# Optimization experiments

Measured on AMD Instinct MI355X. Metric: run time of the kernel, lower is better.

## Reference

```python
import jax, jax.numpy as jnp
import numpy as np
from jax import lax

DIM = 512
MED = 2 * DIM            # expansion_ratio * dim
NF = 4                   # num_filters
SIZE = 64                # spatial size (H = W = size)
FS = SIZE // 2 + 1       # rfft filter size
HR = int(0.5 * DIM)      # reweight hidden (NNConv, 1x1 convs)
HS = int(0.5 * DIM)      # spatial_reweight hidden (Convs, 3x3 convs)
B = 16


def _conv1x1(x, w, b):
    # x: [B,C,H,W], w: [O,C,1,1]
    return jnp.einsum('bchw,oc->bohw', x, w[:, :, 0, 0]) + b[None, :, None, None]


def _conv3x3(x, w, b):
    # x: [B,C,H,W], w: [O,C,3,3], padding=1
    return lax.conv_general_dilated(x, w, (1, 1), 'SAME') + b[None, :, None, None]


def setup_inputs() -> dict:
    key = jax.random.key(0)
    ks = jax.random.split(key, 12)
    n = lambda k, shape, s=0.02: jax.random.normal(k, shape, jnp.float32) * s
    return dict(
        x=jax.random.normal(ks[0], (B, DIM, SIZE, SIZE), jnp.float32),
        w_pw1=n(ks[1], (MED, DIM)),                 # pwconv1 (Linear, no bias)
        w_pw2=n(ks[2], (DIM, MED)),                 # pwconv2 (Linear, no bias)
        star_scale=jnp.ones((1,), jnp.float32),     # StarReLU scale
        star_bias=jnp.zeros((1,), jnp.float32),     # StarReLU bias
        rw_fc1_w=n(ks[3], (HR, DIM, 1, 1)), rw_fc1_b=jnp.zeros((HR,), jnp.float32),
        rw_conv_w=n(ks[4], (HR, HR, 1, 1)), rw_conv_b=jnp.zeros((HR,), jnp.float32),
        rw_fc2_w=n(ks[5], (NF * MED, HR, 1, 1)), rw_fc2_b=jnp.zeros((NF * MED,), jnp.float32),
        sp_fc1_w=n(ks[6], (HS, DIM, 3, 3)), sp_fc1_b=jnp.zeros((HS,), jnp.float32),
        sp_fc2_w=n(ks[7], (NF * MED, HS, 3, 3)), sp_fc2_b=jnp.zeros((NF * MED,), jnp.float32),
        complex_weights=n(ks[8], (SIZE, FS, NF, 2), 0.02),
        spatial_weights=n(ks[9], (SIZE, SIZE, NF), 0.03),
    )


def reference(x, w_pw1, w_pw2, star_scale, star_bias,
              rw_fc1_w, rw_fc1_b, rw_conv_w, rw_conv_b, rw_fc2_w, rw_fc2_b,
              sp_fc1_w, sp_fc1_b, sp_fc2_w, sp_fc2_b,
              complex_weights, spatial_weights):
    Bn, _, H, W = x.shape
    # --- routing branch (NNConv: 1x1 conv -> relu -> 1x1 conv -> relu -> 1x1 conv) ---
    r = jax.nn.relu(_conv1x1(x, rw_fc1_w, rw_fc1_b))
    r = jax.nn.relu(_conv1x1(r, rw_conv_w, rw_conv_b))
    r = _conv1x1(r, rw_fc2_w, rw_fc2_b)                      # [B, NF*MED, H, W]
    routeing = jax.nn.softmax(r.mean(axis=(2, 3)).reshape(Bn, NF, MED), axis=1)
    # --- spatial routing branch (Convs: 3x3 conv -> relu -> 3x3 conv) ---
    s = jax.nn.relu(_conv3x3(x, sp_fc1_w, sp_fc1_b))
    s = _conv3x3(s, sp_fc2_w, sp_fc2_b)                      # [B, NF*MED, H, W]
    spatial_routeing = jax.nn.softmax(s.mean(axis=(2, 3)).reshape(Bn, NF, MED), axis=1)
    # --- main path ---
    xc = jnp.transpose(x, (0, 2, 3, 1))                      # [B,H,W,DIM]
    xp = jnp.einsum('bhwc,mc->bhwm', xc, w_pw1)              # pwconv1 -> [B,H,W,MED]
    xp = star_scale * jnp.square(jax.nn.relu(xp)) + star_bias  # StarReLU
    xf = jnp.fft.rfft2(xp, axes=(1, 2), norm='ortho')        # [B,H,FS,MED] complex64
    cw = lax.complex(complex_weights[..., 0], complex_weights[..., 1])  # [H,FS,NF]
    weight = jnp.einsum('bfc,hwf->bhwc', routeing.astype(cw.dtype), cw)  # [B,H,FS,MED]
    spatial_weight = jnp.einsum('bfc,hwf->bhwc', spatial_routeing, spatial_weights)  # [B,H,W,MED]
    xs = jnp.fft.irfft2(xf * weight, s=(H, W), axes=(1, 2), norm='ortho')
    out = xp * spatial_weight + xs                            # spatial gating + FFT filter
    out = jnp.einsum('bhwm,dm->bhwd', out, w_pw2)             # pwconv2
    return jnp.transpose(out, (0, 3, 1, 2))                   # [B,DIM,H,W]
```

## Files before the change

kernel.cpp:

```cpp
#include <hip/hip_runtime.h>

#define HW    4096
#define DIMC  512
#define MEDC  1024
#define HRC   256
#define HSC   256
#define NBATCH 16

typedef __attribute__((ext_vector_type(8))) short bf16x8;
typedef __attribute__((ext_vector_type(4))) float f32x4;

static const size_t R1_OFF    = 0;
static const size_t XT_OFF    = 8388608;
static const size_t WCONV_OFF = 25165824;
static const size_t WR1_OFF   = 25755648;
static const size_t WRC_OFF   = 25821184;
static const size_t XP_OFF    = 0;
static const size_t WB1_OFF   = 67108864;
static const size_t WB2_OFF   = 67371008;
static const size_t MEAN_OFF  = 67633152;
static const size_t AGG_OFF   = MEAN_OFF + 4096;
static const size_t TAP_OFF   = AGG_OFF + 36864;
static const size_t ROUTE_OFF = TAP_OFF + 36864;
static const size_t SR_OFF    = ROUTE_OFF + 65536;
static const size_t WS_END    = SR_OFF + 65536;

__device__ __forceinline__ unsigned short f2bf(float f) {
  unsigned u = __float_as_uint(f);
  unsigned r = (u + 0x7fffu + ((u >> 16) & 1u)) >> 16;
  return (unsigned short)r;
}

__global__ __launch_bounds__(256) void cvt_bf16(
    const float* __restrict__ src, unsigned short* __restrict__ dst, int n)
{
  int i = blockIdx.x * 256 + threadIdx.x;
  if (i < n) dst[i] = f2bf(src[i]);
}

__global__ __launch_bounds__(256) void xpose_bf16(
    const float* __restrict__ x, unsigned short* __restrict__ xT)
{
  __shared__ unsigned short T[32][33];
  const int tid = threadIdx.x;
  const int p0 = blockIdx.x * 32, c0 = blockIdx.y * 32, bb = blockIdx.z;
#pragma unroll
  for (int i = 0; i < 4; i++) {
    int idx = i * 256 + tid;
    int c_l = idx >> 5, p_l = idx & 31;
    T[c_l][p_l] = f2bf(x[((size_t)(bb * DIMC + c0 + c_l)) * HW + p0 + p_l]);
  }
  __syncthreads();
#pragma unroll
  for (int i = 0; i < 4; i++) {
    int idx = i * 256 + tid;
    int p_l = idx >> 5, c_l = idx & 31;
    xT[((size_t)bb * HW + p0 + p_l) * DIMC + c0 + c_l] = T[c_l][p_l];
  }
}

__global__ __launch_bounds__(256) void wconv_bf16(
    const float* __restrict__ w, unsigned short* __restrict__ wbf)
{
  int idx = blockIdx.x * 256 + threadIdx.x;
  if (idx < HSC * DIMC) {
#pragma unroll
    for (int t = 0; t < 9; t++)
      wbf[(size_t)t * (HSC * DIMC) + idx] = f2bf(w[(size_t)idx * 9 + t]);
  }
}

template<int EPI, int ASRC>
__global__ __launch_bounds__(256) void gemm_bf16(
    const void* __restrict__ Aptr, const unsigned short* __restrict__ Wb,
    const float* __restrict__ bias, float* __restrict__ Cf,
    unsigned short* __restrict__ Cb, float* __restrict__ meansum,
    const float* __restrict__ star_scale, const float* __restrict__ star_bias,
    int K, int Ntot)
{
  __shared__ __align__(16) unsigned short As[128 * 40];
  __shared__ __align__(16) unsigned short Bs[128 * 40];
  const int tid = threadIdx.x;
  const int pix0 = blockIdx.x * 128;
  const int n0g = blockIdx.y * 128;
  const int bb = blockIdx.z;
  const int wid = tid >> 6, lane = tid & 63;
  const int lo = lane & 15, hi = lane >> 4;
  const int wm = wid >> 1, wn = wid & 1;

  f32x4 acc[4][4];
#pragma unroll
  for (int mi = 0; mi < 4; mi++)
#pragma unroll
    for (int ni = 0; ni < 4; ni++) acc[mi][ni] = (f32x4){0.f, 0.f, 0.f, 0.f};

  const int nsteps = K >> 5;
  for (int s = 0; s < nsteps; s++) {
    const int c0 = s * 32;
    if (ASRC == 0) {
      const unsigned short* AT = (const unsigned short*)Aptr;
#pragma unroll
      for (int it = 0; it < 2; it++) {
        int idx = it * 256 + tid;
        int p = idx >> 2, co = (idx & 3) * 8;
        uint4 v = *(const uint4*)&AT[((size_t)bb * HW + pix0 + p) * K + c0 + co];
        *(uint4*)&As[p * 40 + co] = v;
      }
    } else {
      const float* Af = (const float*)Aptr;
#pragma unroll
      for (int it = 0; it < 16; it++) {
        int idx = it * 256 + tid;
        int k_l = idx >> 7, p_l = idx & 127;
        float v = Af[((size_t)bb * K + c0 + k_l) * HW + pix0 + p_l];
        As[p_l * 40 + k_l] = f2bf(v);
      }
    }
#pragma unroll
    for (int it = 0; it < 2; it++) {
      int idx = it * 256 + tid;
      int o = idx >> 2, co = (idx & 3) * 8;
      uint4 v = *(const uint4*)&Wb[(size_t)(n0g + o) * K + c0 + co];
      *(uint4*)&Bs[o * 40 + co] = v;
    }
    __syncthreads();

    bf16x8 a[4], bq[4];
#pragma unroll
    for (int mi = 0; mi < 4; mi++)
      a[mi] = *(const bf16x8*)&As[(wm * 64 + mi * 16 + lo) * 40 + hi * 8];
#pragma unroll
    for (int ni = 0; ni < 4; ni++)
      bq[ni] = *(const bf16x8*)&Bs[(wn * 64 + ni * 16 + lo) * 40 + hi * 8];
#pragma unroll
    for (int mi = 0; mi < 4; mi++)
#pragma unroll
      for (int ni = 0; ni < 4; ni++)
        acc[mi][ni] = __builtin_amdgcn_mfma_f32_16x16x32_bf16(a[mi], bq[ni], acc[mi][ni], 0, 0, 0);
    __syncthreads();
  }

  if (EPI == 3) {
#pragma unroll
    for (int ni = 0; ni < 4; ni++) {
      const int n = n0g + wn * 64 + ni * 16 + lo;
      const float bia = bias[n];
      float T = 0.f;
#pragma unroll
      for (int mi = 0; mi < 4; mi++)
#pragma unroll
        for (int r = 0; r < 4; r++)
          T += fmaxf(acc[mi][ni][r] + bia, 0.f);
      T += __shfl_xor(T, 16);
      T += __shfl_xor(T, 32);
      if (hi == 0) atomicAdd(&meansum[bb * Ntot + n], T);
    }
    return;
  }

  if (EPI == 1) {
#pragma unroll
    for (int ni = 0; ni < 4; ni++) {
      const int n = n0g + wn * 64 + ni * 16 + lo;
      const float bia = bias[n];
#pragma unroll
      for (int mi = 0; mi < 4; mi++)
#pragma unroll
        for (int r = 0; r < 4; r++) {
          const int pix = pix0 + wm * 64 + mi * 16 + hi * 4 + r;
          Cb[((size_t)bb * HW + pix) * Ntot + n] = f2bf(fmaxf(acc[mi][ni][r] + bia, 0.f));
        }
    }
    return;
  }

  float ss = 1.f, sb = 0.f;
  if (EPI == 2) { ss = star_scale[0]; sb = star_bias[0]; }
#pragma unroll
  for (int ni = 0; ni < 4; ni++) {
    const int n = n0g + wn * 64 + ni * 16 + lo;
#pragma unroll
    for (int mi = 0; mi < 4; mi++) {
      const int pixb = pix0 + wm * 64 + mi * 16 + hi * 4;
      float4 v;
      float* vv = (float*)&v;
#pragma unroll
      for (int r = 0; r < 4; r++) {
        float t = acc[mi][ni][r];
        if (EPI == 2) { t = fmaxf(t, 0.f); t = ss * t * t + sb; }
        vv[r] = t;
      }
      *(float4*)&Cf[((size_t)bb * Ntot + n) * HW + pixb] = v;
    }
  }
}

__global__ __launch_bounds__(256) void conv3_mfma(
    const unsigned short* __restrict__ xT, const unsigned short* __restrict__ wbf,
    const float* __restrict__ bias, float* __restrict__ agg)
{
  __shared__ __align__(16) unsigned short As[128 * 40];
  __shared__ __align__(16) unsigned short Bs[128 * 40];
  const int tid = threadIdx.x;
  const int bx = blockIdx.x;
  const int n0g = blockIdx.y * 128;
  const int bb = blockIdx.z;
  const int h0 = bx * 2;
  const int wid = tid >> 6;
  const int lane = tid & 63;
  const int lo = lane & 15, hi = lane >> 4;
  const int wm = wid >> 1;
  const int wn = wid & 1;

  f32x4 acc[4][4];
#pragma unroll
  for (int mi = 0; mi < 4; mi++)
#pragma unroll
    for (int ni = 0; ni < 4; ni++) acc[mi][ni] = (f32x4){0.f, 0.f, 0.f, 0.f};

  for (int s = 0; s < 144; s++) {
    const int t = s >> 4;
    const int c0 = (s & 15) * 32;
    const int di = t / 3 - 1, dj = t % 3 - 1;
#pragma unroll
    for (int it = 0; it < 2; it++) {
      int idx = it * 256 + tid;
      int pix = idx >> 2, co = (idx & 3) * 8;
      int h = h0 + (pix >> 6) + di;
      int col = (pix & 63) + dj;
      uint4 v = make_uint4(0u, 0u, 0u, 0u);
      if (h >= 0 && h < 64 && col >= 0 && col < 64)
        v = *(const uint4*)&xT[((size_t)bb * HW + h * 64 + col) * DIMC + c0 + co];
      *(uint4*)&As[pix * 40 + co] = v;
    }
#pragma unroll
    for (int it = 0; it < 2; it++) {
      int idx = it * 256 + tid;
      int o = idx >> 2, co = (idx & 3) * 8;
      uint4 v = *(const uint4*)&wbf[((size_t)t * (HSC * DIMC)) + (size_t)(n0g + o) * DIMC + c0 + co];
      *(uint4*)&Bs[o * 40 + co] = v;
    }
    __syncthreads();

    bf16x8 a[4], bfr[4];
#pragma unroll
    for (int mi = 0; mi < 4; mi++)
      a[mi] = *(const bf16x8*)&As[(wm * 64 + mi * 16 + lo) * 40 + hi * 8];
#pragma unroll
    for (int ni = 0; ni < 4; ni++)
      bfr[ni] = *(const bf16x8*)&Bs[(wn * 64 + ni * 16 + lo) * 40 + hi * 8];
#pragma unroll
    for (int mi = 0; mi < 4; mi++)
#pragma unroll
      for (int ni = 0; ni < 4; ni++)
        acc[mi][ni] = __builtin_amdgcn_mfma_f32_16x16x32_bf16(a[mi], bfr[ni], acc[mi][ni], 0, 0, 0);
    __syncthreads();
  }

  const int h = h0 + wm;
#pragma unroll
  for (int ni = 0; ni < 4; ni++) {
    const int o = n0g + wn * 64 + ni * 16 + lo;
    const float bia = bias[o];
    float T = 0.f;
#pragma unroll
    for (int mi = 0; mi < 4; mi++)
#pragma unroll
      for (int r = 0; r < 4; r++)
        T += fmaxf(acc[mi][ni][r] + bia, 0.f);
    T += __shfl_xor(T, 16);
    T += __shfl_xor(T, 32);
    float* ag = &agg[((size_t)bb * HSC + o) * 9];
    if (hi == 0) {
      atomicAdd(ag + 0, T);
      if (h == 0)  atomicAdd(ag + 1, T);
      if (h == 63) atomicAdd(ag + 2, T);
      float c0v = fmaxf(acc[0][ni][0] + bia, 0.f);
      atomicAdd(ag + 3, c0v);
      if (h == 0)  atomicAdd(ag + 5, c0v);
      if (h == 63) atomicAdd(ag + 7, c0v);
    }
    if (hi == 3) {
      float cwv = fmaxf(acc[3][ni][3] + bia, 0.f);
      atomicAdd(ag + 4, cwv);
      if (h == 0)  atomicAdd(ag + 6, cwv);
      if (h == 63) atomicAdd(ag + 8, cwv);
    }
  }
}

__global__ void tap_compute(const float* __restrict__ agg, float* __restrict__ tap)
{
  int b = blockIdx.x; int c = threadIdx.x;
  const float* a = &agg[((size_t)b * HSC + c) * 9];
  float T = a[0], R0 = a[1], RH = a[2], C0 = a[3], CW = a[4];
  float s00 = a[5], s0W = a[6], sH0 = a[7], sHW = a[8];
  float* tp = &tap[((size_t)b * HSC + c) * 9];
#pragma unroll
  for (int i = 0; i < 3; i++)
#pragma unroll
    for (int j = 0; j < 3; j++) {
      int di = i - 1, dj = j - 1;
      float v = T;
      if (di == -1) v -= RH; else if (di == 1) v -= R0;
      if (dj == -1) v -= CW; else if (dj == 1) v -= C0;
      if (di == -1 && dj == -1) v += sHW;
      if (di == -1 && dj ==  1) v += sH0;
      if (di ==  1 && dj == -1) v += s0W;
      if (di ==  1 && dj ==  1) v += s00;
      tp[i * 3 + j] = v * (1.f / 4096.f);
    }
}

__global__ __launch_bounds__(256) void route_softmax(
    const float* __restrict__ meansum, const float* __restrict__ W,
    const float* __restrict__ bias, float* __restrict__ route)
{
  __shared__ float mv[HRC];
  int b = blockIdx.y;
  int m = blockIdx.x * 256 + threadIdx.x;
  mv[threadIdx.x] = meansum[b * HRC + threadIdx.x] * (1.f / 4096.f);
  __syncthreads();
  float l[4];
#pragma unroll
  for (int f = 0; f < 4; f++) {
    int o = f * MEDC + m;
    float accv = bias[o];
    const float* wr = &W[(size_t)o * HRC];
    for (int c = 0; c < HRC; c++) accv += wr[c] * mv[c];
    l[f] = accv;
  }
  float mx = fmaxf(fmaxf(l[0], l[1]), fmaxf(l[2], l[3]));
  float e[4], s = 0.f;
#pragma unroll
  for (int f = 0; f < 4; f++) { e[f] = expf(l[f] - mx); s += e[f]; }
  float inv = 1.f / s;
#pragma unroll
  for (int f = 0; f < 4; f++) route[((size_t)b * 4 + f) * MEDC + m] = e[f] * inv;
}

__global__ __launch_bounds__(256) void sproute_softmax(
    const float* __restrict__ tap, const float* __restrict__ W,
    const float* __restrict__ bias, float* __restrict__ sroute)
{
  __shared__ float tv[HSC * 9];
  int b = blockIdx.y;
  int m = blockIdx.x * 256 + threadIdx.x;
#pragma unroll
  for (int i = 0; i < 9; i++) {
    int idx = i * 256 + threadIdx.x;
    tv[idx] = tap[(size_t)b * HSC * 9 + idx];
  }
  __syncthreads();
  float l[4];
#pragma unroll
  for (int f = 0; f < 4; f++) {
    int o = f * MEDC + m;
    float accv = bias[o];
    const float* wr = &W[(size_t)o * HSC * 9];
    for (int ct = 0; ct < HSC * 9; ct++) accv += wr[ct] * tv[ct];
    l[f] = accv;
  }
  float mx = fmaxf(fmaxf(l[0], l[1]), fmaxf(l[2], l[3]));
  float e[4], s = 0.f;
#pragma unroll
  for (int f = 0; f < 4; f++) { e[f] = expf(l[f] - mx); s += e[f]; }
  float inv = 1.f / s;
#pragma unroll
  for (int f = 0; f < 4; f++) sroute[((size_t)b * 4 + f) * MEDC + m] = e[f] * inv;
}

template<int SGN>
__device__ __forceinline__ void dft8(const float* xr, const float* xi, float* Xr, float* Xi) {
  const float S = (float)SGN;
  const float r = 0.70710678118654752440f;
  float t0r = xr[0] + xr[4], t0i = xi[0] + xi[4];
  float t1r = xr[0] - xr[4], t1i = xi[0] - xi[4];
  float t2r = xr[2] + xr[6], t2i = xi[2] + xi[6];
  float t3r = xr[2] - xr[6], t3i = xi[2] - xi[6];
  float E0r = t0r + t2r, E0i = t0i + t2i;
  float E2r = t0r - t2r, E2i = t0i - t2i;
  float E1r = t1r - S * t3i, E1i = t1i + S * t3r;
  float E3r = t1r + S * t3i, E3i = t1i - S * t3r;
  float u0r = xr[1] + xr[5], u0i = xi[1] + xi[5];
  float u1r = xr[1] - xr[5], u1i = xi[1] - xi[5];
  float u2r = xr[3] + xr[7], u2i = xi[3] + xi[7];
  float u3r = xr[3] - xr[7], u3i = xi[3] - xi[7];
  float O0r = u0r + u2r, O0i = u0i + u2i;
  float O2r = u0r - u2r, O2i = u0i - u2i;
  float O1r = u1r - S * u3i, O1i = u1i + S * u3r;
  float O3r = u1r + S * u3i, O3i = u1i - S * u3r;
  float p1r = r * (O1r - S * O1i), p1i = r * (S * O1r + O1i);
  float p2r = -S * O2i,            p2i = S * O2r;
  float p3r = -r * (O3r + S * O3i), p3i = r * (S * O3r - O3i);
  Xr[0] = E0r + O0r; Xi[0] = E0i + O0i;
  Xr[4] = E0r - O0r; Xi[4] = E0i - O0i;
  Xr[1] = E1r + p1r; Xi[1] = E1i + p1i;
  Xr[5] = E1r - p1r; Xi[5] = E1i - p1i;
  Xr[2] = E2r + p2r; Xi[2] = E2i + p2i;
  Xr[6] = E2r - p2r; Xi[6] = E2i - p2i;
  Xr[3] = E3r + p3r; Xi[3] = E3i + p3i;
  Xr[7] = E3r - p3r; Xi[7] = E3i - p3i;
}

__global__ __launch_bounds__(256) void fft_filter(
    float* __restrict__ xp, const float* __restrict__ route,
    const float* __restrict__ sroute, const float* __restrict__ cw,
    const float* __restrict__ spw)
{
  __shared__ float Fr[64][34], Fi[64][34];
  __shared__ float Cr[2176], Ci[2176];
  __shared__ float twc[64], tws[64];
  const int tid = threadIdx.x;
  const int blk = blockIdx.x;
  const int b = blk >> 10;
  const int m = blk & 1023;
  float* img = xp + (size_t)blk * HW;

  if (tid < 64) {
    float ang = (2.f * 3.14159265358979323846f / 64.f) * (float)tid;
    twc[tid] = cosf(ang); tws[tid] = sinf(ang);
  }
  float r4[4], s4[4];
#pragma unroll
  for (int f = 0; f < 4; f++) {
    r4[f] = route[((size_t)b * 4 + f) * MEDC + m] * (1.f / 4096.f);
    s4[f] = sroute[((size_t)b * 4 + f) * MEDC + m];
  }
  __syncthreads();

#pragma unroll
  for (int half = 0; half < 2; half++) {
    {
      const int rh = tid & 31, n2 = tid >> 5;
      const int r = rh + half * 32;
      float xr[8], xi[8], Br[8], Bi[8];
#pragma unroll
      for (int n1 = 0; n1 < 8; n1++) { xr[n1] = img[r * 64 + 8 * n1 + n2]; xi[n1] = 0.f; }
      dft8<-1>(xr, xi, Br, Bi);
#pragma unroll
      for (int k1 = 0; k1 < 8; k1++) {
        int a = n2 * k1;
        float c = twc[a], s = tws[a];
        Cr[rh * 67 + k1 * 8 + n2] = Br[k1] * c + Bi[k1] * s;
        Ci[rh * 67 + k1 * 8 + n2] = Bi[k1] * c - Br[k1] * s;
      }
    }
    __syncthreads();
    {
      const int rh = tid & 31, k1 = tid >> 5;
      const int r = rh + half * 32;
      float xr[8], xi[8], Xr[8], Xi[8];
#pragma unroll
      for (int n2 = 0; n2 < 8; n2++) {
        xr[n2] = Cr[rh * 67 + k1 * 8 + n2];
        xi[n2] = Ci[rh * 67 + k1 * 8 + n2];
      }
      dft8<-1>(xr, xi, Xr, Xi);
      const int kmax = (k1 == 0) ? 5 : 4;
#pragma unroll
      for (int k2 = 0; k2 < 5; k2++) {
        if (k2 < kmax) {
          Fr[r][k1 + 8 * k2] = Xr[k2];
          Fi[r][k1 + 8 * k2] = Xi[k2];
        }
      }
    }
    __syncthreads();
  }

  for (int t = tid; t < 264; t += 256) {
    const int k = t % 33, n2 = t / 33;
    float xr[8], xi[8], Br[8], Bi[8];
#pragma unroll
    for (int n1 = 0; n1 < 8; n1++) { xr[n1] = Fr[8 * n1 + n2][k]; xi[n1] = Fi[8 * n1 + n2][k]; }
    dft8<-1>(xr, xi, Br, Bi);
#pragma unroll
    for (int k1 = 0; k1 < 8; k1++) {
      int a = n2 * k1;
      float c = twc[a], s = tws[a];
      Cr[(k1 * 8 + n2) * 34 + k] = Br[k1] * c + Bi[k1] * s;
      Ci[(k1 * 8 + n2) * 34 + k] = Bi[k1] * c - Br[k1] * s;
    }
  }
  __syncthreads();
  for (int t = tid; t < 264; t += 256) {
    const int k = t % 33, k1 = t / 33;
    float xr[8], xi[8], Xr[8], Xi[8];
#pragma unroll
    for (int n2 = 0; n2 < 8; n2++) {
      xr[n2] = Cr[(k1 * 8 + n2) * 34 + k];
      xi[n2] = Ci[(k1 * 8 + n2) * 34 + k];
    }
    dft8<-1>(xr, xi, Xr, Xi);
#pragma unroll
    for (int k2 = 0; k2 < 8; k2++) {
      const int kh = k1 + 8 * k2;
      const float* cwp = &cw[(size_t)(kh * 33 + k) * 8];
      float wre = r4[0] * cwp[0] + r4[1] * cwp[2] + r4[2] * cwp[4] + r4[3] * cwp[6];
      float wim = r4[0] * cwp[1] + r4[1] * cwp[3] + r4[2] * cwp[5] + r4[3] * cwp[7];
      Fr[kh][k] = Xr[k2] * wre - Xi[k2] * wim;
      Fi[kh][k] = Xr[k2] * wim + Xi[k2] * wre;
    }
  }
  __syncthreads();

  for (int t = tid; t < 264; t += 256) {
    const int k = t % 33, m2 = t / 33;
    float xr[8], xi[8], Br[8], Bi[8];
#pragma unroll
    for (int m1 = 0; m1 < 8; m1++) { xr[m1] = Fr[8 * m1 + m2][k]; xi[m1] = Fi[8 * m1 + m2][k]; }
    dft8<1>(xr, xi, Br, Bi);
#pragma unroll
    for (int h1 = 0; h1 < 8; h1++) {
      int a = m2 * h1;
      float c = twc[a], s = tws[a];
      Cr[(h1 * 8 + m2) * 34 + k] = Br[h1] * c - Bi[h1] * s;
      Ci[(h1 * 8 + m2) * 34 + k] = Bi[h1] * c + Br[h1] * s;
    }
  }
  __syncthreads();
  for (int t = tid; t < 264; t += 256) {
    const int k = t % 33, h1 = t / 33;
    float xr[8], xi[8], Xr[8], Xi[8];
#pragma unroll
    for (int m2 = 0; m2 < 8; m2++) {
      xr[m2] = Cr[(h1 * 8 + m2) * 34 + k];
      xi[m2] = Ci[(h1 * 8 + m2) * 34 + k];
    }
    dft8<1>(xr, xi, Xr, Xi);
#pragma unroll
    for (int h2 = 0; h2 < 8; h2++) {
      Fr[h1 + 8 * h2][k] = Xr[h2];
      Fi[h1 + 8 * h2][k] = Xi[h2];
    }
  }
  __syncthreads();

#pragma unroll
  for (int half = 0; half < 2; half++) {
    {
      const int rh = tid & 31, m2 = tid >> 5;
      const int r = rh + half * 32;
      float xr[8], xi[8], Br[8], Bi[8];
      if (m2 == 0) {
        xr[0] = Fr[r][0];  xi[0] = 0.f;
        xr[4] = Fr[r][32]; xi[4] = 0.f;
      } else {
        xr[0] = 2.f * Fr[r][m2]; xi[0] = 2.f * Fi[r][m2];
        xr[4] = 0.f; xi[4] = 0.f;
      }
#pragma unroll
      for (int m1 = 1; m1 < 4; m1++) {
        xr[m1] = 2.f * Fr[r][8 * m1 + m2];
        xi[m1] = 2.f * Fi[r][8 * m1 + m2];
      }
      xr[5] = 0.f; xi[5] = 0.f; xr[6] = 0.f; xi[6] = 0.f; xr[7] = 0.f; xi[7] = 0.f;
      dft8<1>(xr, xi, Br, Bi);
#pragma unroll
      for (int h1 = 0; h1 < 8; h1++) {
        int a = m2 * h1;
        float c = twc[a], s = tws[a];
        Cr[rh * 67 + h1 * 8 + m2] = Br[h1] * c - Bi[h1] * s;
        Ci[rh * 67 + h1 * 8 + m2] = Bi[h1] * c + Br[h1] * s;
      }
    }
    __syncthreads();
    {
      const int rh = tid & 31, h1 = tid >> 5;
      const int r = rh + half * 32;
      float xr[8], xi[8], Xr[8], Xi[8];
#pragma unroll
      for (int m2 = 0; m2 < 8; m2++) {
        xr[m2] = Cr[rh * 67 + h1 * 8 + m2];
        xi[m2] = Ci[rh * 67 + h1 * 8 + m2];
      }
      dft8<1>(xr, xi, Xr, Xi);
#pragma unroll
      for (int h2 = 0; h2 < 8; h2++) {
        const int w = h1 + 8 * h2;
        const int pix = r * 64 + w;
        float xv = img[pix];
        const float* sp = &spw[(size_t)pix * 4];
        float sw = s4[0] * sp[0] + s4[1] * sp[1] + s4[2] * sp[2] + s4[3] * sp[3];
        img[pix] = xv * sw + Xr[h2];
      }
    }
    __syncthreads();
  }
}

extern "C" void kernel_launch(void* const* d_in, const int* in_sizes, int n_in,
                              void* d_out, int out_size, void* d_ws, size_t ws_size,
                              hipStream_t stream) {
  const float* x          = (const float*)d_in[0];
  const float* w_pw1      = (const float*)d_in[1];
  const float* w_pw2      = (const float*)d_in[2];
  const float* star_scale = (const float*)d_in[3];
  const float* star_bias  = (const float*)d_in[4];
  const float* rw1w = (const float*)d_in[5];
  const float* rw1b = (const float*)d_in[6];
  const float* rwcw = (const float*)d_in[7];
  const float* rwcb = (const float*)d_in[8];
  const float* rw2w = (const float*)d_in[9];
  const float* rw2b = (const float*)d_in[10];
  const float* sp1w = (const float*)d_in[11];
  const float* sp1b = (const float*)d_in[12];
  const float* sp2w = (const float*)d_in[13];
  const float* sp2b = (const float*)d_in[14];
  const float* cw   = (const float*)d_in[15];
  const float* spw  = (const float*)d_in[16];

  if (ws_size < WS_END * sizeof(float)) return;

  float* ws = (float*)d_ws;
  float* xp = ws + XP_OFF;
  unsigned short* r1    = (unsigned short*)(ws + R1_OFF);
  unsigned short* xT    = (unsigned short*)(ws + XT_OFF);
  unsigned short* wconv = (unsigned short*)(ws + WCONV_OFF);
  unsigned short* wr1   = (unsigned short*)(ws + WR1_OFF);
  unsigned short* wrc   = (unsigned short*)(ws + WRC_OFF);
  unsigned short* wb1   = (unsigned short*)(ws + WB1_OFF);
  unsigned short* wb2   = (unsigned short*)(ws + WB2_OFF);
  float* meansum = ws + MEAN_OFF;
  float* agg     = ws + AGG_OFF;
  float* tap     = ws + TAP_OFF;
  float* route   = ws + ROUTE_OFF;
  float* sr      = ws + SR_OFF;
  float* out = (float*)d_out;

  hipMemsetAsync(meansum, 0, (4096 + 36864) * sizeof(float), stream);

  xpose_bf16<<<dim3(128, 16, 16), 256, 0, stream>>>(x, xT);
  wconv_bf16<<<512, 256, 0, stream>>>(sp1w, wconv);
  cvt_bf16<<<2048, 256, 0, stream>>>(w_pw1, wb1, MEDC * DIMC);
  cvt_bf16<<<2048, 256, 0, stream>>>(w_pw2, wb2, DIMC * MEDC);
  cvt_bf16<<<512, 256, 0, stream>>>(rw1w, wr1, HRC * DIMC);
  cvt_bf16<<<256, 256, 0, stream>>>(rwcw, wrc, HRC * HRC);

  gemm_bf16<1, 0><<<dim3(32, 2, 16), 256, 0, stream>>>(
      xT, wr1, rw1b, nullptr, r1, nullptr, nullptr, nullptr, DIMC, HRC);
  gemm_bf16<3, 0><<<dim3(32, 2, 16), 256, 0, stream>>>(
      r1, wrc, rwcb, nullptr, nullptr, meansum, nullptr, nullptr, HRC, HRC);
  route_softmax<<<dim3(4, 16), 256, 0, stream>>>(meansum, rw2w, rw2b, route);

  conv3_mfma<<<dim3(32, 2, 16), 256, 0, stream>>>(xT, wconv, sp1b, agg);
  tap_compute<<<16, 256, 0, stream>>>(agg, tap);
  sproute_softmax<<<dim3(4, 16), 256, 0, stream>>>(tap, sp2w, sp2b, sr);

  gemm_bf16<2, 1><<<dim3(32, 8, 16), 256, 0, stream>>>(
      x, wb1, nullptr, xp, nullptr, nullptr, star_scale, star_bias, DIMC, MEDC);
  fft_filter<<<16384, 256, 0, stream>>>(xp, route, sr, cw, spw);
  gemm_bf16<0, 1><<<dim3(32, 4, 16), 256, 0, stream>>>(
      xp, wb2, nullptr, out, nullptr, nullptr, nullptr, nullptr, MEDC, DIMC);
}
```

Measured before the change: 1.727 ms.

## Restructure FFT filter to one wavefront with register-resident 64-point FFTs

Rewrites the per-image FFT filter so a single 64-thread wave handles each image, with every lane holding a full 64-point row or column in registers and running a register-only 8x8 decomposition. The old version used 256 threads, separate real/imag shared arrays and many intermediate shared round-trips. The new one keeps only one float2 spectrum buffer in shared memory and uses vectorized float4 global loads and stores. This cuts barriers and shared traffic, but needs about 128+ registers per thread, which may spill or limit occupancy. In the column pass only 33 of 64 lanes do work, so half the wave idles.

New measurement: 2.280 ms. +32.0%, slower.

```diff
diff --git a/kernel.cpp b/kernel.cpp
--- a/kernel.cpp
+++ b/kernel.cpp
@@ -403,23 +403,70 @@
   Xr[7] = E3r - p3r; Xi[7] = E3i - p3i;
 }
 
-__global__ __launch_bounds__(256) void fft_filter(
+template<int SGN>
+__device__ __forceinline__ void dft8_strided(float* xr, float* xi, const int base, const int stride) {
+  float ar[8], ai[8], Br[8], Bi[8];
+#pragma unroll
+  for (int j = 0; j < 8; j++) { ar[j] = xr[base + j * stride]; ai[j] = xi[base + j * stride]; }
+  dft8<SGN>(ar, ai, Br, Bi);
+#pragma unroll
+  for (int j = 0; j < 8; j++) { xr[base + j * stride] = Br[j]; xi[base + j * stride] = Bi[j]; }
+}
+
+template<int SGN>
+__device__ __forceinline__ void fft64_n2r(float* xr, float* xi, const float2* tw) {
+#pragma unroll
+  for (int g = 0; g < 8; g++) dft8_strided<SGN>(xr, xi, g, 8);
+#pragma unroll
+  for (int s = 0; s < 64; s++) {
+    const int a = (s >> 3) * (s & 7);
+    if (a) {
+      float2 t = tw[a];
+      float c = t.x, si = (float)SGN * t.y;
+      float rr = xr[s] * c - xi[s] * si;
+      xi[s] = xr[s] * si + xi[s] * c;
+      xr[s] = rr;
+    }
+  }
+#pragma unroll
+  for (int g = 0; g < 8; g++) dft8_strided<SGN>(xr, xi, 8 * g, 1);
+}
+
+template<int SGN>
+__device__ __forceinline__ void fft64_r2n(float* xr, float* xi, const float2* tw) {
+#pragma unroll
+  for (int g = 0; g < 8; g++) dft8_strided<SGN>(xr, xi, 8 * g, 1);
+#pragma unroll
+  for (int s = 0; s < 64; s++) {
+    const int a = (s >> 3) * (s & 7);
+    if (a) {
+      float2 t = tw[a];
+      float c = t.x, si = (float)SGN * t.y;
+      float rr = xr[s] * c - xi[s] * si;
+      xi[s] = xr[s] * si + xi[s] * c;
+      xr[s] = rr;
+    }
+  }
+#pragma unroll
+  for (int g = 0; g < 8; g++) dft8_strided<SGN>(xr, xi, g, 8);
+}
+
+__global__ __launch_bounds__(64, 2) void fft_filter(
     float* __restrict__ xp, const float* __restrict__ route,
     const float* __restrict__ sroute, const float* __restrict__ cw,
     const float* __restrict__ spw)
 {
-  __shared__ float Fr[64][34], Fi[64][34];
-  __shared__ float Cr[2176], Ci[2176];
-  __shared__ float twc[64], tws[64];
-  const int tid = threadIdx.x;
+  __shared__ float2 Fs[64 * 33];
+  __shared__ float2 tw[64];
+  const int lane = threadIdx.x;
   const int blk = blockIdx.x;
   const int b = blk >> 10;
   const int m = blk & 1023;
   float* img = xp + (size_t)blk * HW;
 
-  if (tid < 64) {
-    float ang = (2.f * 3.14159265358979323846f / 64.f) * (float)tid;
-    twc[tid] = cosf(ang); tws[tid] = sinf(ang);
+  {
+    float ang = (6.28318530717958647693f / 64.f) * (float)lane;
+    tw[lane] = make_float2(cosf(ang), sinf(ang));
   }
   float r4[4], s4[4];
 #pragma unroll
@@ -429,164 +476,75 @@
   }
   __syncthreads();
 
-#pragma unroll
-  for (int half = 0; half < 2; half++) {
-    {
-      const int rh = tid & 31, n2 = tid >> 5;
-      const int r = rh + half * 32;
-      float xr[8], xi[8], Br[8], Bi[8];
-#pragma unroll
-      for (int n1 = 0; n1 < 8; n1++) { xr[n1] = img[r * 64 + 8 * n1 + n2]; xi[n1] = 0.f; }
-      dft8<-1>(xr, xi, Br, Bi);
-#pragma unroll
-      for (int k1 = 0; k1 < 8; k1++) {
-        int a = n2 * k1;
-        float c = twc[a], s = tws[a];
-        Cr[rh * 67 + k1 * 8 + n2] = Br[k1] * c + Bi[k1] * s;
-        Ci[rh * 67 + k1 * 8 + n2] = Bi[k1] * c - Br[k1] * s;
-      }
-    }
-    __syncthreads();
-    {
-      const int rh = tid & 31, k1 = tid >> 5;
-      const int r = rh + half * 32;
-      float xr[8], xi[8], Xr[8], Xi[8];
-#pragma unroll
-      for (int n2 = 0; n2 < 8; n2++) {
-        xr[n2] = Cr[rh * 67 + k1 * 8 + n2];
-        xi[n2] = Ci[rh * 67 + k1 * 8 + n2];
-      }
-      dft8<-1>(xr, xi, Xr, Xi);
-      const int kmax = (k1 == 0) ? 5 : 4;
-#pragma unroll
-      for (int k2 = 0; k2 < 5; k2++) {
-        if (k2 < kmax) {
-          Fr[r][k1 + 8 * k2] = Xr[k2];
-          Fi[r][k1 + 8 * k2] = Xi[k2];
-        }
-      }
-    }
-    __syncthreads();
-  }
-
-  for (int t = tid; t < 264; t += 256) {
-    const int k = t % 33, n2 = t / 33;
-    float xr[8], xi[8], Br[8], Bi[8];
-#pragma unroll
-    for (int n1 = 0; n1 < 8; n1++) { xr[n1] = Fr[8 * n1 + n2][k]; xi[n1] = Fi[8 * n1 + n2][k]; }
-    dft8<-1>(xr, xi, Br, Bi);
-#pragma unroll
-    for (int k1 = 0; k1 < 8; k1++) {
-      int a = n2 * k1;
-      float c = twc[a], s = tws[a];
-      Cr[(k1 * 8 + n2) * 34 + k] = Br[k1] * c + Bi[k1] * s;
-      Ci[(k1 * 8 + n2) * 34 + k] = Bi[k1] * c - Br[k1] * s;
-    }
-  }
+  float xr[64], xi[64];
+
+#pragma unroll
+  for (int t = 0; t < 16; t++) {
+    float4 v = *(const float4*)&img[lane * 64 + t * 4];
+    xr[4 * t + 0] = v.x; xr[4 * t + 1] = v.y; xr[4 * t + 2] = v.z; xr[4 * t + 3] = v.w;
+    xi[4 * t + 0] = 0.f; xi[4 * t + 1] = 0.f; xi[4 * t + 2] = 0.f; xi[4 * t + 3] = 0.f;
+  }
+  fft64_n2r<-1>(xr, xi, tw);
+#pragma unroll
+  for (int k1 = 0; k1 < 8; k1++)
+#pragma unroll
+    for (int k2 = 0; k2 < 5; k2++) {
+      const int k = k1 + 8 * k2;
+      if (k <= 32)
+        Fs[lane * 33 + k] = make_float2(xr[8 * k1 + k2], xi[8 * k1 + k2]);
+    }
   __syncthreads();
-  for (int t = tid; t < 264; t += 256) {
-    const int k = t % 33, k1 = t / 33;
-    float xr[8], xi[8], Xr[8], Xi[8];
-#pragma unroll
-    for (int n2 = 0; n2 < 8; n2++) {
-      xr[n2] = Cr[(k1 * 8 + n2) * 34 + k];
-      xi[n2] = Ci[(k1 * 8 + n2) * 34 + k];
-    }
-    dft8<-1>(xr, xi, Xr, Xi);
-#pragma unroll
-    for (int k2 = 0; k2 < 8; k2++) {
-      const int kh = k1 + 8 * k2;
-      const float* cwp = &cw[(size_t)(kh * 33 + k) * 8];
-      float wre = r4[0] * cwp[0] + r4[1] * cwp[2] + r4[2] * cwp[4] + r4[3] * cwp[6];
-      float wim = r4[0] * cwp[1] + r4[1] * cwp[3] + r4[2] * cwp[5] + r4[3] * cwp[7];
-      Fr[kh][k] = Xr[k2] * wre - Xi[k2] * wim;
-      Fi[kh][k] = Xr[k2] * wim + Xi[k2] * wre;
-    }
+
+  if (lane < 33) {
+#pragma unroll
+    for (int h = 0; h < 64; h++) {
+      float2 v = Fs[h * 33 + lane];
+      xr[h] = v.x; xi[h] = v.y;
+    }
+    fft64_n2r<-1>(xr, xi, tw);
+#pragma unroll
+    for (int s = 0; s < 64; s++) {
+      const int kh = (s >> 3) + 8 * (s & 7);
+      const float* cwp = &cw[(size_t)(kh * 33 + lane) * 8];
+      float4 c0 = *(const float4*)cwp;
+      float4 c1 = *(const float4*)(cwp + 4);
+      float wre = r4[0] * c0.x + r4[1] * c0.z + r4[2] * c1.x + r4[3] * c1.z;
+      float wim = r4[0] * c0.y + r4[1] * c0.w + r4[2] * c1.y + r4[3] * c1.w;
+      float rr = xr[s] * wre - xi[s] * wim;
+      xi[s] = xr[s] * wim + xi[s] * wre;
+      xr[s] = rr;
+    }
+    fft64_r2n<1>(xr, xi, tw);
+#pragma unroll
+    for (int h = 0; h < 64; h++)
+      Fs[h * 33 + lane] = make_float2(xr[h], xi[h]);
   }
   __syncthreads();
 
-  for (int t = tid; t < 264; t += 256) {
-    const int k = t % 33, m2 = t / 33;
-    float xr[8], xi[8], Br[8], Bi[8];
-#pragma unroll
-    for (int m1 = 0; m1 < 8; m1++) { xr[m1] = Fr[8 * m1 + m2][k]; xi[m1] = Fi[8 * m1 + m2][k]; }
-    dft8<1>(xr, xi, Br, Bi);
-#pragma unroll
-    for (int h1 = 0; h1 < 8; h1++) {
-      int a = m2 * h1;
-      float c = twc[a], s = tws[a];
-      Cr[(h1 * 8 + m2) * 34 + k] = Br[h1] * c - Bi[h1] * s;
-      Ci[(h1 * 8 + m2) * 34 + k] = Bi[h1] * c + Br[h1] * s;
-    }
-  }
-  __syncthreads();
-  for (int t = tid; t < 264; t += 256) {
-    const int k = t % 33, h1 = t / 33;
-    float xr[8], xi[8], Xr[8], Xi[8];
-#pragma unroll
-    for (int m2 = 0; m2 < 8; m2++) {
-      xr[m2] = Cr[(h1 * 8 + m2) * 34 + k];
-      xi[m2] = Ci[(h1 * 8 + m2) * 34 + k];
-    }
-    dft8<1>(xr, xi, Xr, Xi);
-#pragma unroll
-    for (int h2 = 0; h2 < 8; h2++) {
-      Fr[h1 + 8 * h2][k] = Xr[h2];
-      Fi[h1 + 8 * h2][k] = Xi[h2];
-    }
-  }
-  __syncthreads();
-
-#pragma unroll
-  for (int half = 0; half < 2; half++) {
-    {
-      const int rh = tid & 31, m2 = tid >> 5;
-      const int r = rh + half * 32;
-      float xr[8], xi[8], Br[8], Bi[8];
-      if (m2 == 0) {
-        xr[0] = Fr[r][0];  xi[0] = 0.f;
-        xr[4] = Fr[r][32]; xi[4] = 0.f;
-      } else {
-        xr[0] = 2.f * Fr[r][m2]; xi[0] = 2.f * Fi[r][m2];
-        xr[4] = 0.f; xi[4] = 0.f;
-      }
-#pragma unroll
-      for (int m1 = 1; m1 < 4; m1++) {
-        xr[m1] = 2.f * Fr[r][8 * m1 + m2];
-        xi[m1] = 2.f * Fi[r][8 * m1 + m2];
-      }
-      xr[5] = 0.f; xi[5] = 0.f; xr[6] = 0.f; xi[6] = 0.f; xr[7] = 0.f; xi[7] = 0.f;
-      dft8<1>(xr, xi, Br, Bi);
-#pragma unroll
-      for (int h1 = 0; h1 < 8; h1++) {
-        int a = m2 * h1;
-        float c = twc[a], s = tws[a];
-        Cr[rh * 67 + h1 * 8 + m2] = Br[h1] * c - Bi[h1] * s;
-        Ci[rh * 67 + h1 * 8 + m2] = Bi[h1] * c + Br[h1] * s;
-      }
-    }
-    __syncthreads();
-    {
-      const int rh = tid & 31, h1 = tid >> 5;
-      const int r = rh + half * 32;
-      float xr[8], xi[8], Xr[8], Xi[8];
-#pragma unroll
-      for (int m2 = 0; m2 < 8; m2++) {
-        xr[m2] = Cr[rh * 67 + h1 * 8 + m2];
-        xi[m2] = Ci[rh * 67 + h1 * 8 + m2];
-      }
-      dft8<1>(xr, xi, Xr, Xi);
-#pragma unroll
-      for (int h2 = 0; h2 < 8; h2++) {
-        const int w = h1 + 8 * h2;
-        const int pix = r * 64 + w;
-        float xv = img[pix];
-        const float* sp = &spw[(size_t)pix * 4];
-        float sw = s4[0] * sp[0] + s4[1] * sp[1] + s4[2] * sp[2] + s4[3] * sp[3];
-        img[pix] = xv * sw + Xr[h2];
-      }
-    }
-    __syncthreads();
+#pragma unroll
+  for (int k = 0; k < 33; k++) {
+    float2 v = Fs[lane * 33 + k];
+    if (k == 0 || k == 32) { xr[k] = v.x; xi[k] = 0.f; }
+    else                   { xr[k] = 2.f * v.x; xi[k] = 2.f * v.y; }
+  }
+#pragma unroll
+  for (int k = 33; k < 64; k++) { xr[k] = 0.f; xi[k] = 0.f; }
+  fft64_n2r<1>(xr, xi, tw);
+#pragma unroll
+  for (int t = 0; t < 16; t++) {
+    float4 xv = *(const float4*)&img[lane * 64 + t * 4];
+    const float* xvp = (const float*)&xv;
+    float4 ov;
+    float* ovp = (float*)&ov;
+#pragma unroll
+    for (int j = 0; j < 4; j++) {
+      const int w = 4 * t + j;
+      const int s = 8 * (w & 7) + (w >> 3);
+      float4 sp = *(const float4*)&spw[(size_t)(lane * 64 + w) * 4];
+      float sw = s4[0] * sp.x + s4[1] * sp.y + s4[2] * sp.z + s4[3] * sp.w;
+      ovp[j] = xvp[j] * sw + xr[s];
+    }
+    *(float4*)&img[lane * 64 + t * 4] = ov;
   }
 }
 
@@ -650,7 +608,7 @@
 
   gemm_bf16<2, 1><<<dim3(32, 8, 16), 256, 0, stream>>>(
       x, wb1, nullptr, xp, nullptr, nullptr, star_scale, star_bias, DIMC, MEDC);
-  fft_filter<<<16384, 256, 0, stream>>>(xp, route, sr, cw, spw);
+  fft_filter<<<16384, 64, 0, stream>>>(xp, route, sr, cw, spw);
   gemm_bf16<0, 1><<<dim3(32, 4, 16), 256, 0, stream>>>(
       xp, wb2, nullptr, out, nullptr, nullptr, nullptr, nullptr, MEDC, DIMC);
 }
```
